# Performance work log

Hardware: AMD Instinct MI355X
Metric: run time of the kernel (lower is better)

## Reference

```python
import jax, jax.numpy as jnp
import numpy as np

N_NODES = 100000
N_EDGES = 3200000


def setup_inputs() -> dict:
    key = jax.random.key(0)
    ks = jax.random.split(key, 12)
    inp = {
        "x": jax.random.normal(ks[0], (N_NODES, 4), dtype=jnp.float32),
        "edge": jax.random.randint(ks[1], (2, N_EDGES), 0, N_NODES, dtype=jnp.int64),
        "weight": jax.random.uniform(ks[2], (N_EDGES,), dtype=jnp.float32),
        "W1": jax.random.normal(ks[3], (8, 4), dtype=jnp.float32) * 0.5,
        "b1": jax.random.normal(ks[4], (8,), dtype=jnp.float32) * 0.1,
        "W3": jax.random.normal(ks[5], (16, 8), dtype=jnp.float32) * 0.35,
        "b3": jax.random.normal(ks[6], (16,), dtype=jnp.float32) * 0.1,
        "W5": jax.random.normal(ks[7], (32, 16), dtype=jnp.float32) * 0.25,
        "b5": jax.random.normal(ks[8], (32,), dtype=jnp.float32) * 0.1,
        "W7": jax.random.normal(ks[9], (2, 32), dtype=jnp.float32) * 0.18,
        "b7": jax.random.normal(ks[10], (2,), dtype=jnp.float32) * 0.1,
    }
    return inp


def reference(x, edge, weight, W1, b1, W3, b3, W5, b5, W7, b7):
    row, col = edge[0], edge[1]
    n = x.shape[0]
    lrelu = jax.nn.leaky_relu  # default negative_slope=0.01, same as torch
    # per-row edge counts for scatter_mean (rows with 0 edges -> 0, like torch_scatter)
    cnt = jax.ops.segment_sum(jnp.ones_like(weight), row, num_segments=n)
    inv_cnt = jnp.where(cnt > 0, 1.0 / jnp.maximum(cnt, 1.0), 0.0)[:, None]

    def block(h, W, b):
        msg = h[col] * weight[:, None]          # gather + edge-weight scale [E,F]
        msg = lrelu(msg @ W.T + b)              # per-edge Linear + LeakyReLU
        agg = jax.ops.segment_sum(msg, row, num_segments=n) * inv_cnt  # scatter_mean
        return agg + lrelu(h @ W.T + b)         # residual branch

    h = block(x, W1, b1)   # [N,8]
    h = block(h, W3, b3)   # [N,16]
    h = block(h, W5, b5)   # [N,32]
    pooled = jnp.mean(h, axis=0, keepdims=True)  # global_mean_pool (single graph) [1,32]
    logits = pooled @ W7.T + b7                  # [1,2]
    return jax.nn.log_softmax(logits, axis=1)
```

## Files before the change

### kernel.cpp

```cpp
#include <hip/hip_runtime.h>
#include <hip/hip_bf16.h>
#include <math.h>


#define LB256 __launch_bounds__(256)

#define NB_SHIFT 8
#define NB_ROWS  (1 << NB_SHIFT)
#define GA 512
#define TILE 2048
#define CBCAP 12288

template <int PT>
__global__ LB256 void gscan_sum(const int* __restrict__ a, int n, int* __restrict__ bsum) {
    int base = blockIdx.x * (256 * PT);
    int sum = 0;
    for (int i = threadIdx.x; i < 256 * PT; i += 256) {
        int idx = base + i;
        sum += (idx < n) ? a[idx] : 0;
    }
#pragma unroll
    for (int o = 32; o; o >>= 1) sum += __shfl_down(sum, o);
    __shared__ int ws[4];
    if ((threadIdx.x & 63) == 0) ws[threadIdx.x >> 6] = sum;
    __syncthreads();
    if (threadIdx.x == 0) bsum[blockIdx.x] = ws[0] + ws[1] + ws[2] + ws[3];
}

__global__ void gscan_offsets(const int* __restrict__ bsum, int nbk, int* __restrict__ boff) {
    int lane = threadIdx.x;
    int v = (lane < nbk) ? bsum[lane] : 0;
    int orig = v;
#pragma unroll
    for (int o = 1; o < 64; o <<= 1) {
        int u = __shfl_up(v, o);
        if (lane >= o) v += u;
    }
    if (lane < nbk) boff[lane] = v - orig;
}

template <int PT>
__global__ LB256 void gscan_scatter(const int* __restrict__ a, int n,
                                    const int* __restrict__ boff, int total,
                                    int* __restrict__ out1) {
    int base = blockIdx.x * (256 * PT);
    int idx0 = base + threadIdx.x * PT;
    int vals[PT];
    int s = 0;
#pragma unroll
    for (int k = 0; k < PT; ++k) {
        int id = idx0 + k;
        vals[k] = (id < n) ? a[id] : 0;
        s += vals[k];
    }
    int lane = threadIdx.x & 63, wid = threadIdx.x >> 6;
    int inc = s;
#pragma unroll
    for (int o = 1; o < 64; o <<= 1) {
        int u = __shfl_up(inc, o);
        if (lane >= o) inc += u;
    }
    __shared__ int wsum[4];
    if (lane == 63) wsum[wid] = inc;
    __syncthreads();
    int woff = 0;
    for (int i = 0; i < wid; ++i) woff += wsum[i];
    int excl = inc - s + woff + boff[blockIdx.x];
#pragma unroll
    for (int k = 0; k < PT; ++k) {
        int id = idx0 + k;
        if (id < n) out1[id] = excl;
        excl += vals[k];
    }
    if (blockIdx.x == 0 && threadIdx.x == 0) out1[n] = total;
}


__global__ LB256 void hist_kernel(const int* __restrict__ row, int E, int nb, int chunk,
                                  int* __restrict__ countmat) {
    __shared__ int lh[512];
    for (int b = threadIdx.x; b < 512; b += 256) lh[b] = 0;
    __syncthreads();
    int beg = blockIdx.x * chunk;
    int end = min(E, beg + chunk);
    for (int i = beg + threadIdx.x; i < end; i += 256)
        atomicAdd(&lh[row[i] >> NB_SHIFT], 1);
    __syncthreads();
    for (int b = threadIdx.x; b < nb; b += 256)
        countmat[b * gridDim.x + blockIdx.x] = lh[b];
}

__global__ LB256 void sort_scatter_kernel(const int* __restrict__ row, const int* __restrict__ col,
                                          const float* __restrict__ w, const int* __restrict__ off,
                                          int E, int G, int chunk,
                                          unsigned long long* __restrict__ tmp) {
    __shared__ unsigned long long stage[TILE];
    __shared__ int lh[512];
    __shared__ int seg[512];
    __shared__ int gcur[512];
    __shared__ int wsum[4];
    int blk = blockIdx.x, tid = threadIdx.x;
    int beg = blk * chunk, end = min(E, beg + chunk);
    for (int b = tid; b < 512; b += 256) {
        gcur[b] = off[b * G + blk];
        lh[b] = 0;
    }
    __syncthreads();

    for (int tbase = beg; tbase < end; tbase += TILE) {
        int tcnt = min(TILE, end - tbase);
        int bk[8], sl[8];
        unsigned long long en[8];
#pragma unroll
        for (int k = 0; k < 8; ++k) {
            int e = tbase + k * 256 + tid;
            bk[k] = -1;
            if (e < end) {
                int r = row[e];
                int b = r >> NB_SHIFT;
                unsigned wb = (__float_as_uint(w[e]) + 0x8000u) >> 16;
                en[k] = ((unsigned long long)b << 40) |
                        ((unsigned long long)(r & (NB_ROWS - 1)) << 32) |
                        (unsigned long long)((wb << 17) | (unsigned)col[e]);
                bk[k] = b;
                sl[k] = atomicAdd(&lh[b], 1);
            }
        }
        __syncthreads();
        int c0 = lh[2 * tid], c1 = lh[2 * tid + 1];
        int tsum = c0 + c1;
        int lane = tid & 63, wid = tid >> 6;
        int inc = tsum;
#pragma unroll
        for (int o = 1; o < 64; o <<= 1) {
            int u = __shfl_up(inc, o);
            if (lane >= o) inc += u;
        }
        if (lane == 63) wsum[wid] = inc;
        __syncthreads();
        int woff = 0;
        for (int i = 0; i < wid; ++i) woff += wsum[i];
        int ex = inc - tsum + woff;
        seg[2 * tid] = ex;
        seg[2 * tid + 1] = ex + c0;
        __syncthreads();
#pragma unroll
        for (int k = 0; k < 8; ++k)
            if (bk[k] >= 0) stage[seg[bk[k]] + sl[k]] = en[k];
        __syncthreads();
        for (int p = tid; p < tcnt; p += 256) {
            unsigned long long ent = stage[p];
            int b = (int)(ent >> 40);
            tmp[gcur[b] + (p - seg[b])] = ent;
        }
        __syncthreads();
        for (int b = tid; b < 512; b += 256) {
            gcur[b] += lh[b];
            lh[b] = 0;
        }
        __syncthreads();
    }
}

__global__ LB256 void csr_build_kernel(const unsigned long long* __restrict__ tmp,
                                       const int* __restrict__ off,
                                       int G, int N, int E,
                                       int* __restrict__ rowptr, unsigned* __restrict__ csr) {
    __shared__ int lcnt[NB_ROWS];
    __shared__ int wsum[4];
    __shared__ unsigned stage[CBCAP];
    int b = blockIdx.x;
    int tid = threadIdx.x;
    int s0 = off[b * G];
    int e0 = off[(b + 1) * G];
    int seg = e0 - s0;
    int rbase = b << NB_SHIFT;

    lcnt[tid] = 0;
    __syncthreads();
    for (int j = s0 + tid; j < e0; j += 256)
        atomicAdd(&lcnt[(int)((tmp[j] >> 32) & 0xFFu)], 1);
    __syncthreads();

    int val = lcnt[tid];
    int lane = tid & 63, wid = tid >> 6;
    int inc = val;
#pragma unroll
    for (int o = 1; o < 64; o <<= 1) {
        int u = __shfl_up(inc, o);
        if (lane >= o) inc += u;
    }
    if (lane == 63) wsum[wid] = inc;
    __syncthreads();
    int woff = 0;
    for (int i = 0; i < wid; ++i) woff += wsum[i];
    int ex = inc - val + woff;

    int idx = rbase + tid;
    if (idx < N) rowptr[idx] = s0 + ex;
    if (b == gridDim.x - 1 && tid == 0) rowptr[N] = E;
    __syncthreads();
    lcnt[tid] = ex;
    __syncthreads();

    if (seg <= CBCAP) {
        for (int j = s0 + tid; j < e0; j += 256) {
            unsigned long long ent = tmp[j];
            int pos = atomicAdd(&lcnt[(int)((ent >> 32) & 0xFFu)], 1);
            stage[pos] = (unsigned)ent;
        }
        __syncthreads();
        for (int p = tid; p < seg; p += 256) csr[s0 + p] = stage[p];
    } else {
        for (int j = s0 + tid; j < e0; j += 256) {
            unsigned long long ent = tmp[j];
            int pos = s0 + atomicAdd(&lcnt[(int)((ent >> 32) & 0xFFu)], 1);
            csr[pos] = (unsigned)ent;
        }
    }
}


template <int FIN, int FOUT>
__global__ LB256 void transform_kernel(const float* __restrict__ h, const float* __restrict__ W,
                                       __hip_bfloat16* __restrict__ t0,
                                       __hip_bfloat16* __restrict__ t1, int n) {
    constexpr int FH = (FOUT > 16) ? 16 : FOUT;
    int i = blockIdx.x * blockDim.x + threadIdx.x;
    if (i >= n * FOUT) return;
    int v = i / FOUT;
    int f = i % FOUT;
    float s = 0.0f;
#pragma unroll
    for (int k = 0; k < FIN; ++k) s = fmaf(h[v * FIN + k], W[f * FIN + k], s);
    __hip_bfloat16 bv = __float2bfloat16(s);
    if (f < FH) t0[v * FH + f] = bv;
    else        t1[v * FH + (f - FH)] = bv;
}

template <int GS, int FTOT>
__global__ LB256 void agg_half_kernel(const int* __restrict__ rowptr,
                                      const unsigned* __restrict__ csr,
                                      const unsigned* __restrict__ th,
                                      const float* __restrict__ b, int fo,
                                      float* __restrict__ h, int N) {
    constexpr int RPB = 256 / GS;
    int g = threadIdx.x / GS;
    int l = threadIdx.x % GS;
    int v = blockIdx.x * RPB + g;
    if (v >= N) return;
    int beg = rowptr[v], end = rowptr[v + 1];
    float bf0 = b[fo + 2 * l];
    float bf1 = b[fo + 2 * l + 1];
    float a0 = 0.0f, a1 = 0.0f;

    int j = beg;
    for (; j + 15 < end; j += 16) {
        unsigned e[16];
#pragma unroll
        for (int u = 0; u < 16; ++u) e[u] = __builtin_nontemporal_load(&csr[j + u]);
        unsigned tv[16];
#pragma unroll
        for (int u = 0; u < 16; ++u) tv[u] = th[(e[u] & 0x1FFFFu) * GS + l];
#pragma unroll
        for (int u = 0; u < 16; ++u) {
            float wv = __uint_as_float((e[u] & 0xFFFE0000u) >> 1);
            float m0 = fmaf(wv, __uint_as_float(tv[u] << 16), bf0);
            float m1 = fmaf(wv, __uint_as_float(tv[u] & 0xffff0000u), bf1);
            a0 += (m0 > 0.f) ? m0 : 0.01f * m0;
            a1 += (m1 > 0.f) ? m1 : 0.01f * m1;
        }
    }
    for (; j + 3 < end; j += 4) {
        unsigned e[4];
#pragma unroll
        for (int u = 0; u < 4; ++u) e[u] = __builtin_nontemporal_load(&csr[j + u]);
        unsigned tv[4];
#pragma unroll
        for (int u = 0; u < 4; ++u) tv[u] = th[(e[u] & 0x1FFFFu) * GS + l];
#pragma unroll
        for (int u = 0; u < 4; ++u) {
            float wv = __uint_as_float((e[u] & 0xFFFE0000u) >> 1);
            float m0 = fmaf(wv, __uint_as_float(tv[u] << 16), bf0);
            float m1 = fmaf(wv, __uint_as_float(tv[u] & 0xffff0000u), bf1);
            a0 += (m0 > 0.f) ? m0 : 0.01f * m0;
            a1 += (m1 > 0.f) ? m1 : 0.01f * m1;
        }
    }
    for (; j < end; ++j) {
        unsigned e0 = __builtin_nontemporal_load(&csr[j]);
        unsigned t0 = th[(e0 & 0x1FFFFu) * GS + l];
        float wv = __uint_as_float((e0 & 0xFFFE0000u) >> 1);
        float m0 = fmaf(wv, __uint_as_float(t0 << 16), bf0);
        float m1 = fmaf(wv, __uint_as_float(t0 & 0xffff0000u), bf1);
        a0 += (m0 > 0.f) ? m0 : 0.01f * m0;
        a1 += (m1 > 0.f) ? m1 : 0.01f * m1;
    }

    int deg = end - beg;
    float iv = deg ? 1.0f / (float)deg : 0.0f;
    unsigned tr = th[v * GS + l];
    float r0 = __uint_as_float(tr << 16) + bf0;
    float r1 = __uint_as_float(tr & 0xffff0000u) + bf1;
    r0 = (r0 > 0.f) ? r0 : 0.01f * r0;
    r1 = (r1 > 0.f) ? r1 : 0.01f * r1;
    float2 st = make_float2(fmaf(a0, iv, r0), fmaf(a1, iv, r1));
    *(float2*)(h + (size_t)v * FTOT + fo + 2 * l) = st;
}


__global__ LB256 void pool_kernel(const float* __restrict__ h, float* __restrict__ pool, int n) {
    __shared__ float ls[256];
    int f = threadIdx.x & 31;
    int grp = threadIdx.x >> 5;
    int gid = blockIdx.x * (blockDim.x >> 5) + grp;
    int ngrp = (blockDim.x >> 5) * gridDim.x;
    float s = 0.0f;
    for (int v = gid; v < n; v += ngrp) s += h[v * 32 + f];
    ls[threadIdx.x] = s;
    __syncthreads();
    if (threadIdx.x < 32) {
        float tot = 0.0f;
#pragma unroll
        for (int g = 0; g < 8; ++g) tot += ls[g * 32 + threadIdx.x];
        atomicAdd(&pool[threadIdx.x], tot);
    }
}

__global__ void head_kernel(const float* __restrict__ pool, const float* __restrict__ W7,
                            const float* __restrict__ b7, float* __restrict__ out, int n) {
    if (threadIdx.x != 0 || blockIdx.x != 0) return;
    float invn = 1.0f / (float)n;
    float l0 = b7[0], l1 = b7[1];
    for (int f = 0; f < 32; ++f) {
        float p = pool[f] * invn;
        l0 = fmaf(p, W7[f], l0);
        l1 = fmaf(p, W7[32 + f], l1);
    }
    float m = fmaxf(l0, l1);
    float lse = m + logf(expf(l0 - m) + expf(l1 - m));
    out[0] = l0 - lse;
    out[1] = l1 - lse;
}


extern "C" void kernel_launch(void* const* d_in, const int* in_sizes, int n_in,
                              void* d_out, int out_size, void* d_ws, size_t ws_size,
                              hipStream_t stream) {
    const float* x  = (const float*)d_in[0];
    const int* edge = (const int*)d_in[1];
    const float* w  = (const float*)d_in[2];
    const float* W1 = (const float*)d_in[3];
    const float* b1 = (const float*)d_in[4];
    const float* W3 = (const float*)d_in[5];
    const float* b3 = (const float*)d_in[6];
    const float* W5 = (const float*)d_in[7];
    const float* b5 = (const float*)d_in[8];
    const float* W7 = (const float*)d_in[9];
    const float* b7 = (const float*)d_in[10];
    float* out = (float*)d_out;

    const int N = in_sizes[0] / 4;
    const int E = in_sizes[1] / 2;
    const int* row = edge;
    const int* col = edge + E;

    const int nb = (N + NB_ROWS - 1) >> NB_SHIFT;
    const int G = GA;
    const int chunk = (E + G - 1) / G;
    const int M = nb * G;

    char* ws = (char*)d_ws;
    size_t off8 = 0;
    auto alloc = [&](size_t bytes) {
        void* p = ws + off8;
        off8 += (bytes + 255) & ~(size_t)255;
        return p;
    };
    int*      bsum     = (int*)alloc(256 * 4);
    int*      boff     = (int*)alloc(256 * 4);
    int*      countmat = (int*)alloc((size_t)M * 4);
    int*      offm     = (int*)alloc(((size_t)M + 1) * 4);
    int*      rowptr   = (int*)alloc(((size_t)N + 1) * 4);
    float*    pool     = (float*)alloc(32 * 4);
    unsigned* csr      = (unsigned*)alloc((size_t)E * 4);
    __hip_bfloat16* t0 = (__hip_bfloat16*)alloc((size_t)N * 16 * 2);
    __hip_bfloat16* t1 = (__hip_bfloat16*)alloc((size_t)N * 16 * 2);
    float*    h1       = (float*)alloc((size_t)N * 8 * 4);
    float*    h2       = (float*)alloc((size_t)N * 16 * 4);
    size_t tmpsz = (size_t)E * 8;
    size_t h3sz  = (size_t)N * 32 * 4;
    char*  big   = (char*)alloc(tmpsz > h3sz ? tmpsz : h3sz);
    unsigned long long* tmp = (unsigned long long*)big;
    float*              h3  = (float*)big;
    (void)ws_size;

    hipMemsetAsync(pool, 0, 32 * 4, stream);

    const int B = 256;
    const int nbkM = (M + 4095) / 4096;

    hist_kernel<<<G, B, 0, stream>>>(row, E, nb, chunk, countmat);
    gscan_sum<16><<<nbkM, B, 0, stream>>>(countmat, M, bsum);
    gscan_offsets<<<1, 64, 0, stream>>>(bsum, nbkM, boff);
    gscan_scatter<16><<<nbkM, B, 0, stream>>>(countmat, M, boff, E, offm);
    sort_scatter_kernel<<<G, B, 0, stream>>>(row, col, w, offm, E, G, chunk, tmp);
    csr_build_kernel<<<nb, B, 0, stream>>>(tmp, offm, G, N, E, rowptr, csr);

    transform_kernel<4, 8><<<(N * 8 + B - 1) / B, B, 0, stream>>>(x, W1, t0, t0, N);
    agg_half_kernel<4, 8><<<(N + 63) / 64, B, 0, stream>>>(rowptr, csr, (const unsigned*)t0, b1, 0, h1, N);

    transform_kernel<8, 16><<<(N * 16 + B - 1) / B, B, 0, stream>>>(h1, W3, t0, t0, N);
    agg_half_kernel<8, 16><<<(N + 31) / 32, B, 0, stream>>>(rowptr, csr, (const unsigned*)t0, b3, 0, h2, N);

    transform_kernel<16, 32><<<(N * 32 + B - 1) / B, B, 0, stream>>>(h2, W5, t0, t1, N);
    agg_half_kernel<8, 32><<<(N + 31) / 32, B, 0, stream>>>(rowptr, csr, (const unsigned*)t0, b5, 0, h3, N);
    agg_half_kernel<8, 32><<<(N + 31) / 32, B, 0, stream>>>(rowptr, csr, (const unsigned*)t1, b5, 16, h3, N);

    pool_kernel<<<256, B, 0, stream>>>(h3, pool, N);
    head_kernel<<<1, 64, 0, stream>>>(pool, W7, b7, out, N);
}
```

Before: 354.3 us.

## Widen aggregation to 4 features per lane, enlarge CSR-build blocks and scan tiles

The aggregation kernel now loads 8-byte packed bf16 quads per lane, so each lane handles four features and each row uses half as many lanes. This means more rows per block and fewer redundant CSR index loads per row. The CSR build kernel runs with 512 threads, the scan kernels process 32 elements per thread, and GA is doubled. The intent is to cut per-edge index traffic and launch/occupancy overhead, at the cost of less lane parallelism per row and more registers.

Measured after the change: 383.3 us. 8.2% more time.

```diff
diff --git a/kernel.cpp b/kernel.cpp
--- a/kernel.cpp
+++ b/kernel.cpp
@@ -2,12 +2,11 @@
 #include <hip/hip_bf16.h>
 #include <math.h>
 
-
 #define LB256 __launch_bounds__(256)
 
 #define NB_SHIFT 8
 #define NB_ROWS  (1 << NB_SHIFT)
-#define GA 512
+#define GA 1024
 #define TILE 2048
 #define CBCAP 12288
 
@@ -162,10 +161,11 @@
     }
 }
 
-__global__ LB256 void csr_build_kernel(const unsigned long long* __restrict__ tmp,
-                                       const int* __restrict__ off,
-                                       int G, int N, int E,
-                                       int* __restrict__ rowptr, unsigned* __restrict__ csr) {
+__global__ __launch_bounds__(512) void csr_build_kernel(const unsigned long long* __restrict__ tmp,
+                                                        const int* __restrict__ off,
+                                                        int G, int N, int E,
+                                                        int* __restrict__ rowptr,
+                                                        unsigned* __restrict__ csr) {
     __shared__ int lcnt[NB_ROWS];
     __shared__ int wsum[4];
     __shared__ unsigned stage[CBCAP];
@@ -176,43 +176,46 @@
     int seg = e0 - s0;
     int rbase = b << NB_SHIFT;
 
-    lcnt[tid] = 0;
-    __syncthreads();
-    for (int j = s0 + tid; j < e0; j += 256)
+    if (tid < NB_ROWS) lcnt[tid] = 0;
+    __syncthreads();
+    for (int j = s0 + tid; j < e0; j += 512)
         atomicAdd(&lcnt[(int)((tmp[j] >> 32) & 0xFFu)], 1);
     __syncthreads();
 
-    int val = lcnt[tid];
+    int val = 0, inc = 0;
     int lane = tid & 63, wid = tid >> 6;
-    int inc = val;
-#pragma unroll
-    for (int o = 1; o < 64; o <<= 1) {
-        int u = __shfl_up(inc, o);
-        if (lane >= o) inc += u;
-    }
-    if (lane == 63) wsum[wid] = inc;
-    __syncthreads();
-    int woff = 0;
-    for (int i = 0; i < wid; ++i) woff += wsum[i];
-    int ex = inc - val + woff;
-
-    int idx = rbase + tid;
-    if (idx < N) rowptr[idx] = s0 + ex;
+    if (tid < NB_ROWS) {
+        val = lcnt[tid];
+        inc = val;
+#pragma unroll
+        for (int o = 1; o < 64; o <<= 1) {
+            int u = __shfl_up(inc, o);
+            if (lane >= o) inc += u;
+        }
+        if (lane == 63) wsum[wid] = inc;
+    }
+    __syncthreads();
+    if (tid < NB_ROWS) {
+        int woff = 0;
+        for (int i = 0; i < wid; ++i) woff += wsum[i];
+        int ex = inc - val + woff;
+        int idx = rbase + tid;
+        if (idx < N) rowptr[idx] = s0 + ex;
+        lcnt[tid] = ex;
+    }
     if (b == gridDim.x - 1 && tid == 0) rowptr[N] = E;
     __syncthreads();
-    lcnt[tid] = ex;
-    __syncthreads();
 
     if (seg <= CBCAP) {
-        for (int j = s0 + tid; j < e0; j += 256) {
+        for (int j = s0 + tid; j < e0; j += 512) {
             unsigned long long ent = tmp[j];
             int pos = atomicAdd(&lcnt[(int)((ent >> 32) & 0xFFu)], 1);
             stage[pos] = (unsigned)ent;
         }
         __syncthreads();
-        for (int p = tid; p < seg; p += 256) csr[s0 + p] = stage[p];
+        for (int p = tid; p < seg; p += 512) csr[s0 + p] = stage[p];
     } else {
-        for (int j = s0 + tid; j < e0; j += 256) {
+        for (int j = s0 + tid; j < e0; j += 512) {
             unsigned long long ent = tmp[j];
             int pos = s0 + atomicAdd(&lcnt[(int)((ent >> 32) & 0xFFu)], 1);
             csr[pos] = (unsigned)ent;
@@ -238,74 +241,71 @@
     else        t1[v * FH + (f - FH)] = bv;
 }
 
-template <int GS, int FTOT>
+template <int FH, int FTOT>
 __global__ LB256 void agg_half_kernel(const int* __restrict__ rowptr,
                                       const unsigned* __restrict__ csr,
-                                      const unsigned* __restrict__ th,
+                                      const unsigned long long* __restrict__ th,
                                       const float* __restrict__ b, int fo,
                                       float* __restrict__ h, int N) {
+    constexpr int GS = FH / 4;
     constexpr int RPB = 256 / GS;
     int g = threadIdx.x / GS;
     int l = threadIdx.x % GS;
     int v = blockIdx.x * RPB + g;
     if (v >= N) return;
     int beg = rowptr[v], end = rowptr[v + 1];
-    float bf0 = b[fo + 2 * l];
-    float bf1 = b[fo + 2 * l + 1];
-    float a0 = 0.0f, a1 = 0.0f;
+    float bf0 = b[fo + 4 * l + 0];
+    float bf1 = b[fo + 4 * l + 1];
+    float bf2 = b[fo + 4 * l + 2];
+    float bf3 = b[fo + 4 * l + 3];
+    float a0 = 0.f, a1 = 0.f, a2 = 0.f, a3 = 0.f;
 
     int j = beg;
     for (; j + 15 < end; j += 16) {
         unsigned e[16];
 #pragma unroll
         for (int u = 0; u < 16; ++u) e[u] = __builtin_nontemporal_load(&csr[j + u]);
-        unsigned tv[16];
+        unsigned long long tv[16];
 #pragma unroll
         for (int u = 0; u < 16; ++u) tv[u] = th[(e[u] & 0x1FFFFu) * GS + l];
 #pragma unroll
         for (int u = 0; u < 16; ++u) {
             float wv = __uint_as_float((e[u] & 0xFFFE0000u) >> 1);
-            float m0 = fmaf(wv, __uint_as_float(tv[u] << 16), bf0);
-            float m1 = fmaf(wv, __uint_as_float(tv[u] & 0xffff0000u), bf1);
-            a0 += (m0 > 0.f) ? m0 : 0.01f * m0;
-            a1 += (m1 > 0.f) ? m1 : 0.01f * m1;
-        }
-    }
-    for (; j + 3 < end; j += 4) {
-        unsigned e[4];
-#pragma unroll
-        for (int u = 0; u < 4; ++u) e[u] = __builtin_nontemporal_load(&csr[j + u]);
-        unsigned tv[4];
-#pragma unroll
-        for (int u = 0; u < 4; ++u) tv[u] = th[(e[u] & 0x1FFFFu) * GS + l];
-#pragma unroll
-        for (int u = 0; u < 4; ++u) {
-            float wv = __uint_as_float((e[u] & 0xFFFE0000u) >> 1);
-            float m0 = fmaf(wv, __uint_as_float(tv[u] << 16), bf0);
-            float m1 = fmaf(wv, __uint_as_float(tv[u] & 0xffff0000u), bf1);
-            a0 += (m0 > 0.f) ? m0 : 0.01f * m0;
-            a1 += (m1 > 0.f) ? m1 : 0.01f * m1;
+            unsigned lo = (unsigned)tv[u], hi = (unsigned)(tv[u] >> 32);
+            float m;
+            m = fmaf(wv, __uint_as_float(lo << 16), bf0);          a0 += (m > 0.f) ? m : 0.01f * m;
+            m = fmaf(wv, __uint_as_float(lo & 0xffff0000u), bf1);  a1 += (m > 0.f) ? m : 0.01f * m;
+            m = fmaf(wv, __uint_as_float(hi << 16), bf2);          a2 += (m > 0.f) ? m : 0.01f * m;
+            m = fmaf(wv, __uint_as_float(hi & 0xffff0000u), bf3);  a3 += (m > 0.f) ? m : 0.01f * m;
         }
     }
     for (; j < end; ++j) {
         unsigned e0 = __builtin_nontemporal_load(&csr[j]);
-        unsigned t0 = th[(e0 & 0x1FFFFu) * GS + l];
+        unsigned long long tv = th[(e0 & 0x1FFFFu) * GS + l];
         float wv = __uint_as_float((e0 & 0xFFFE0000u) >> 1);
-        float m0 = fmaf(wv, __uint_as_float(t0 << 16), bf0);
-        float m1 = fmaf(wv, __uint_as_float(t0 & 0xffff0000u), bf1);
-        a0 += (m0 > 0.f) ? m0 : 0.01f * m0;
-        a1 += (m1 > 0.f) ? m1 : 0.01f * m1;
+        unsigned lo = (unsigned)tv, hi = (unsigned)(tv >> 32);
+        float m;
+        m = fmaf(wv, __uint_as_float(lo << 16), bf0);          a0 += (m > 0.f) ? m : 0.01f * m;
+        m = fmaf(wv, __uint_as_float(lo & 0xffff0000u), bf1);  a1 += (m > 0.f) ? m : 0.01f * m;
+        m = fmaf(wv, __uint_as_float(hi << 16), bf2);          a2 += (m > 0.f) ? m : 0.01f * m;
+        m = fmaf(wv, __uint_as_float(hi & 0xffff0000u), bf3);  a3 += (m > 0.f) ? m : 0.01f * m;
     }
 
     int deg = end - beg;
     float iv = deg ? 1.0f / (float)deg : 0.0f;
-    unsigned tr = th[v * GS + l];
-    float r0 = __uint_as_float(tr << 16) + bf0;
-    float r1 = __uint_as_float(tr & 0xffff0000u) + bf1;
+    unsigned long long tr = th[(size_t)v * GS + l];
+    unsigned lo = (unsigned)tr, hi = (unsigned)(tr >> 32);
+    float r0 = __uint_as_float(lo << 16) + bf0;
+    float r1 = __uint_as_float(lo & 0xffff0000u) + bf1;
+    float r2 = __uint_as_float(hi << 16) + bf2;
+    float r3 = __uint_as_float(hi & 0xffff0000u) + bf3;
     r0 = (r0 > 0.f) ? r0 : 0.01f * r0;
     r1 = (r1 > 0.f) ? r1 : 0.01f * r1;
-    float2 st = make_float2(fmaf(a0, iv, r0), fmaf(a1, iv, r1));
-    *(float2*)(h + (size_t)v * FTOT + fo + 2 * l) = st;
+    r2 = (r2 > 0.f) ? r2 : 0.01f * r2;
+    r3 = (r3 > 0.f) ? r3 : 0.01f * r3;
+    float4 st = make_float4(fmaf(a0, iv, r0), fmaf(a1, iv, r1),
+                            fmaf(a2, iv, r2), fmaf(a3, iv, r3));
+    *(float4*)(h + (size_t)v * FTOT + fo + 4 * l) = st;
 }
 
 
@@ -398,24 +398,24 @@
     hipMemsetAsync(pool, 0, 32 * 4, stream);
 
     const int B = 256;
-    const int nbkM = (M + 4095) / 4096;
+    const int nbkM = (M + 8191) / 8192;
 
     hist_kernel<<<G, B, 0, stream>>>(row, E, nb, chunk, countmat);
-    gscan_sum<16><<<nbkM, B, 0, stream>>>(countmat, M, bsum);
+    gscan_sum<32><<<nbkM, B, 0, stream>>>(countmat, M, bsum);
     gscan_offsets<<<1, 64, 0, stream>>>(bsum, nbkM, boff);
-    gscan_scatter<16><<<nbkM, B, 0, stream>>>(countmat, M, boff, E, offm);
+    gscan_scatter<32><<<nbkM, B, 0, stream>>>(countmat, M, boff, E, offm);
     sort_scatter_kernel<<<G, B, 0, stream>>>(row, col, w, offm, E, G, chunk, tmp);
-    csr_build_kernel<<<nb, B, 0, stream>>>(tmp, offm, G, N, E, rowptr, csr);
+    csr_build_kernel<<<nb, 512, 0, stream>>>(tmp, offm, G, N, E, rowptr, csr);
 
     transform_kernel<4, 8><<<(N * 8 + B - 1) / B, B, 0, stream>>>(x, W1, t0, t0, N);
-    agg_half_kernel<4, 8><<<(N + 63) / 64, B, 0, stream>>>(rowptr, csr, (const unsigned*)t0, b1, 0, h1, N);
+    agg_half_kernel<8, 8><<<(N + 127) / 128, B, 0, stream>>>(rowptr, csr, (const unsigned long long*)t0, b1, 0, h1, N);
 
     transform_kernel<8, 16><<<(N * 16 + B - 1) / B, B, 0, stream>>>(h1, W3, t0, t0, N);
-    agg_half_kernel<8, 16><<<(N + 31) / 32, B, 0, stream>>>(rowptr, csr, (const unsigned*)t0, b3, 0, h2, N);
+    agg_half_kernel<16, 16><<<(N + 63) / 64, B, 0, stream>>>(rowptr, csr, (const unsigned long long*)t0, b3, 0, h2, N);
 
     transform_kernel<16, 32><<<(N * 32 + B - 1) / B, B, 0, stream>>>(h2, W5, t0, t1, N);
-    agg_half_kernel<8, 32><<<(N + 31) / 32, B, 0, stream>>>(rowptr, csr, (const unsigned*)t0, b5, 0, h3, N);
-    agg_half_kernel<8, 32><<<(N + 31) / 32, B, 0, stream>>>(rowptr, csr, (const unsigned*)t1, b5, 16, h3, N);
+    agg_half_kernel<16, 32><<<(N + 63) / 64, B, 0, stream>>>(rowptr, csr, (const unsigned long long*)t0, b5, 0, h3, N);
+    agg_half_kernel<16, 32><<<(N + 63) / 64, B, 0, stream>>>(rowptr, csr, (const unsigned long long*)t1, b5, 16, h3, N);
 
     pool_kernel<<<256, B, 0, stream>>>(h3, pool, N);
     head_kernel<<<1, 64, 0, stream>>>(pool, W7, b7, out, N);
```
